# Kernel optimization log

Measured on AMD Instinct MI355X. Metric: run time of the kernel, lower is better.

## Reference

```python
import jax, jax.numpy as jnp
import numpy as np

LOG2_HASHMAP_SIZE = 19
HASHMAP_MASK = np.uint32((1 << LOG2_HASHMAP_SIZE) - 1)
# num_mf_layers=4 -> mf_layer_indices=[2,5,8,11] of the 12-level geometric
# resolution list between base=16 and finest=512
RESOLUTIONS = (30, 80, 210, 512)
PRIMES = (np.uint32(1), np.uint32(11614769), np.uint32(2654435761))
N_POINTS = 2_000_000
N_FEATS = 2

# 8 corner offsets of a 3D voxel, shape [8, 3]
CORNER_OFFSETS = jnp.array([[i, j, k] for i in (0, 1) for j in (0, 1) for k in (0, 1)], dtype=jnp.int32)


def _hash3(coords):
    # coords: [..., 3] int32 grid coordinates -> [...] int32 hash index
    c = coords.astype(jnp.uint32)
    h = (c[..., 0] * PRIMES[0]) ^ (c[..., 1] * PRIMES[1]) ^ (c[..., 2] * PRIMES[2])
    return (h & HASHMAP_MASK).astype(jnp.int32)


def setup_inputs() -> dict:
    key = jax.random.key(0)
    k1, k2 = jax.random.split(key)
    # points inside the unit bounding box
    x = jax.random.uniform(k1, (N_POINTS, 3), dtype=jnp.float32)
    # 4 hash tables, init U(-1e-4, 1e-4) as in nn.init.uniform_
    tables = jax.random.uniform(k2, (len(RESOLUTIONS), 1 << LOG2_HASHMAP_SIZE, N_FEATS),
                                minval=-1e-4, maxval=1e-4, dtype=jnp.float32)
    return {"x": x, "tables": tables}


def reference(x, tables):
    # x: [N, 3] in [0, 1]; tables: [L, 2^19, F]
    outs = []
    for li, res in enumerate(RESOLUTIONS):
        scaled = x * jnp.float32(res)          # [N, 3]
        bottom = jnp.floor(scaled)             # voxel min vertex
        t = scaled - bottom                    # relative position in voxel, [N, 3]
        corners = bottom.astype(jnp.int32)[:, None, :] + CORNER_OFFSETS[None]  # [N, 8, 3]
        idx = _hash3(corners)                  # [N, 8]
        emb = tables[li][idx]                  # gather corner embeddings, [N, 8, F]
        # trilinear weights: prod over dims of (t if offset==1 else 1-t)
        w = jnp.where(CORNER_OFFSETS[None].astype(bool), t[:, None, :], 1.0 - t[:, None, :]).prod(axis=-1)  # [N, 8]
        outs.append(jnp.einsum('nc,ncf->nf', w, emb))  # [N, F]
    return jnp.concatenate(outs, axis=-1)  # [N, L*F] = [N, 8]
```

## Files before the change

kernel.cpp:

```cpp
#include <hip/hip_runtime.h>
#include <stdint.h>

#define LOG2_HASHMAP_SIZE 19
#define HASHMAP_SIZE (1u << LOG2_HASHMAP_SIZE)
#define HASHMAP_MASK (HASHMAP_SIZE - 1u)
#define N_LEVELS 4

__device__ __forceinline__ float2 level_embed_p(float px, float py, float pz,
                                                const float* __restrict__ tables,
                                                int li, float r)
{
    const uint32_t P1 = 11614769u;
    const uint32_t P2 = 2654435761u;

    const float sx = px * r, sy = py * r, sz = pz * r;
    const float bx = floorf(sx), by = floorf(sy), bz = floorf(sz);
    const float tx = sx - bx, ty = sy - by, tz = sz - bz;
    const float ux = 1.0f - tx, uy = 1.0f - ty, uz = 1.0f - tz;

    const uint32_t ix = (uint32_t)(int)bx;
    const uint32_t iy = (uint32_t)(int)by;
    const uint32_t iz = (uint32_t)(int)bz;

    const uint32_t hy0 = iy * P1, hy1 = (iy + 1u) * P1;
    const uint32_t hz0 = iz * P2, hz1 = (iz + 1u) * P2;

    uint32_t S[4];
    float W[4];
    S[0] = hy0 ^ hz0;  W[0] = uy * uz;
    S[1] = hy0 ^ hz1;  W[1] = uy * tz;
    S[2] = hy1 ^ hz0;  W[2] = ty * uz;
    S[3] = hy1 ^ hz1;  W[3] = ty * tz;

    const float* tab = tables + (size_t)li * HASHMAP_SIZE * 2;
    const float2* __restrict__ tab2 = (const float2*)tab;
    const float4* __restrict__ tab4 = (const float4*)tab;

    float f0 = 0.0f, f1 = 0.0f;

    if ((ix & 1u) == 0u) {
        #pragma unroll
        for (int c = 0; c < 4; ++c) {
            const uint32_t h0 = (ix ^ S[c]) & HASHMAP_MASK;
            const float4 v = tab4[h0 >> 1];
            const bool hi = (h0 & 1u);
            const float e0x = hi ? v.z : v.x;
            const float e0y = hi ? v.w : v.y;
            const float e1x = hi ? v.x : v.z;
            const float e1y = hi ? v.y : v.w;
            f0 += W[c] * (ux * e0x + tx * e1x);
            f1 += W[c] * (ux * e0y + tx * e1y);
        }
    } else {
        #pragma unroll
        for (int c = 0; c < 4; ++c) {
            const uint32_t h0 = (ix ^ S[c]) & HASHMAP_MASK;
            const uint32_t h1 = ((ix + 1u) ^ S[c]) & HASHMAP_MASK;
            const float2 e0 = tab2[h0];
            const float2 e1 = tab2[h1];
            f0 += W[c] * (ux * e0.x + tx * e1.x);
            f1 += W[c] * (ux * e0.y + tx * e1.y);
        }
    }
    return make_float2(f0, f1);
}

__global__ __launch_bounds__(256) void pass_ws_kernel(
    const float* __restrict__ x, const float* __restrict__ tables,
    float2* __restrict__ ws, int li, float r, int n)
{
    const int i = blockIdx.x * blockDim.x + threadIdx.x;
    if (i >= n) return;
    const float px = x[3 * (size_t)i + 0];
    const float py = x[3 * (size_t)i + 1];
    const float pz = x[3 * (size_t)i + 2];
    ws[i] = level_embed_p(px, py, pz, tables, li, r);
}

__global__ __launch_bounds__(256) void final_kernel(
    const float* __restrict__ x, const float* __restrict__ tables,
    const float2* __restrict__ ws0, const float2* __restrict__ ws1,
    const float2* __restrict__ ws2, float* __restrict__ out, int n)
{
    const int i = blockIdx.x * blockDim.x + threadIdx.x;
    if (i >= n) return;
    const float px = x[3 * (size_t)i + 0];
    const float py = x[3 * (size_t)i + 1];
    const float pz = x[3 * (size_t)i + 2];
    const float2 e3 = level_embed_p(px, py, pz, tables, 3, 512.0f);
    const float2 e0 = ws0[i];
    const float2 e1 = ws1[i];
    const float2 e2 = ws2[i];
    float4* op = (float4*)(out + 8 * (size_t)i);
    op[0] = make_float4(e0.x, e0.y, e1.x, e1.y);
    op[1] = make_float4(e2.x, e2.y, e3.x, e3.y);
}

__global__ __launch_bounds__(256) void pass_direct_kernel(
    const float* __restrict__ x, const float* __restrict__ tables,
    float* __restrict__ out, int li, float r, int n)
{
    const int i = blockIdx.x * blockDim.x + threadIdx.x;
    if (i >= n) return;
    const float px = x[3 * (size_t)i + 0];
    const float py = x[3 * (size_t)i + 1];
    const float pz = x[3 * (size_t)i + 2];
    const float2 e = level_embed_p(px, py, pz, tables, li, r);
    float2* op = (float2*)(out + 8 * (size_t)i + 2 * li);
    *op = e;
}

extern "C" void kernel_launch(void* const* d_in, const int* in_sizes, int n_in,
                              void* d_out, int out_size, void* d_ws, size_t ws_size,
                              hipStream_t stream) {
    const float* x = (const float*)d_in[0];
    const float* tables = (const float*)d_in[1];
    float* out = (float*)d_out;
    const int n = in_sizes[0] / 3;

    const float res[N_LEVELS] = {30.0f, 80.0f, 210.0f, 512.0f};
    const int block = 256;
    const int grid = (n + block - 1) / block;

    const size_t ws_needed = 3 * (size_t)n * sizeof(float2);
    if (ws_size >= ws_needed) {
        float2* ws = (float2*)d_ws;
        for (int li = 0; li < 3; ++li) {
            pass_ws_kernel<<<grid, block, 0, stream>>>(
                x, tables, ws + (size_t)li * n, li, res[li], n);
        }
        final_kernel<<<grid, block, 0, stream>>>(
            x, tables, ws, ws + (size_t)n, ws + 2 * (size_t)n, out, n);
    } else {
        for (int li = 0; li < N_LEVELS; ++li) {
            pass_direct_kernel<<<grid, block, 0, stream>>>(
                x, tables, out, li, res[li], n);
        }
    }
}
```

Before: 284.2 us.

## Fuse all levels into one persistent kernel with fp16 dense level-0 grid in LDS

Result: slower. 347.7 us (+22.3%).

```diff
diff --git a/kernel.cpp b/kernel.cpp
--- a/kernel.cpp
+++ b/kernel.cpp
@@ -1,10 +1,21 @@
 #include <hip/hip_runtime.h>
+#include <hip/hip_fp16.h>
 #include <stdint.h>
 
 #define LOG2_HASHMAP_SIZE 19
 #define HASHMAP_SIZE (1u << LOG2_HASHMAP_SIZE)
 #define HASHMAP_MASK (HASHMAP_SIZE - 1u)
 #define N_LEVELS 4
+
+#define R0 31
+#define DENSE0_N (R0 * R0 * R0)
+#define DENSE0_BYTES (DENSE0_N * 4)
+
+typedef float v4f __attribute__((ext_vector_type(4)));
+
+__device__ __forceinline__ uint32_t hash3(uint32_t ix, uint32_t iy, uint32_t iz) {
+    return (ix ^ (iy * 11614769u) ^ (iz * 2654435761u)) & HASHMAP_MASK;
+}
 
 __device__ __forceinline__ float2 level_embed_p(float px, float py, float pz,
                                                 const float* __restrict__ tables,
@@ -65,35 +76,71 @@
     return make_float2(f0, f1);
 }
 
-__global__ __launch_bounds__(256) void pass_ws_kernel(
-    const float* __restrict__ x, const float* __restrict__ tables,
-    float2* __restrict__ ws, int li, float r, int n)
+__global__ __launch_bounds__(256) void build_dense0(
+    const float* __restrict__ tables, uint32_t* __restrict__ dense0)
 {
-    const int i = blockIdx.x * blockDim.x + threadIdx.x;
-    if (i >= n) return;
-    const float px = x[3 * (size_t)i + 0];
-    const float py = x[3 * (size_t)i + 1];
-    const float pz = x[3 * (size_t)i + 2];
-    ws[i] = level_embed_p(px, py, pz, tables, li, r);
+    const int v = blockIdx.x * blockDim.x + threadIdx.x;
+    if (v >= DENSE0_N) return;
+    const int vx = v / (R0 * R0);
+    const int rem = v - vx * (R0 * R0);
+    const int vy = rem / R0;
+    const int vz = rem - vy * R0;
+    const uint32_t h = hash3((uint32_t)vx, (uint32_t)vy, (uint32_t)vz);
+    const float2 e = ((const float2*)tables)[h];
+    const __half2 p = __floats2half2_rn(e.x, e.y);
+    dense0[v] = *(const uint32_t*)&p;
 }
 
-__global__ __launch_bounds__(256) void final_kernel(
+extern __shared__ uint32_t s_dense[];
+
+__global__ __launch_bounds__(1024) void fused_kernel(
     const float* __restrict__ x, const float* __restrict__ tables,
-    const float2* __restrict__ ws0, const float2* __restrict__ ws1,
-    const float2* __restrict__ ws2, float* __restrict__ out, int n)
+    const uint32_t* __restrict__ dense0, float* __restrict__ out, int n)
 {
-    const int i = blockIdx.x * blockDim.x + threadIdx.x;
-    if (i >= n) return;
-    const float px = x[3 * (size_t)i + 0];
-    const float py = x[3 * (size_t)i + 1];
-    const float pz = x[3 * (size_t)i + 2];
-    const float2 e3 = level_embed_p(px, py, pz, tables, 3, 512.0f);
-    const float2 e0 = ws0[i];
-    const float2 e1 = ws1[i];
-    const float2 e2 = ws2[i];
-    float4* op = (float4*)(out + 8 * (size_t)i);
-    op[0] = make_float4(e0.x, e0.y, e1.x, e1.y);
-    op[1] = make_float4(e2.x, e2.y, e3.x, e3.y);
+    for (int i = threadIdx.x; i < DENSE0_N; i += 1024)
+        s_dense[i] = dense0[i];
+    __syncthreads();
+
+    const size_t stride = (size_t)gridDim.x * 1024;
+    for (size_t i = (size_t)blockIdx.x * 1024 + threadIdx.x; i < (size_t)n; i += stride) {
+        const float px = __builtin_nontemporal_load(x + 3 * i + 0);
+        const float py = __builtin_nontemporal_load(x + 3 * i + 1);
+        const float pz = __builtin_nontemporal_load(x + 3 * i + 2);
+
+        const float2 e1 = level_embed_p(px, py, pz, tables, 1, 80.0f);
+        const float2 e2 = level_embed_p(px, py, pz, tables, 2, 210.0f);
+        const float2 e3 = level_embed_p(px, py, pz, tables, 3, 512.0f);
+
+        const float sx = px * 30.0f, sy = py * 30.0f, sz = pz * 30.0f;
+        const float bx = floorf(sx), by = floorf(sy), bz = floorf(sz);
+        const float tx = sx - bx, ty = sy - by, tz = sz - bz;
+        const float uxv = 1.0f - tx, uyv = 1.0f - ty, uzv = 1.0f - tz;
+        const int ix = (int)bx, iy = (int)by, iz = (int)bz;
+        const int lin = (ix * R0 + iy) * R0 + iz;
+
+        float f0 = 0.0f, f1 = 0.0f;
+        #pragma unroll
+        for (int dx = 0; dx < 2; ++dx) {
+            const float wx = dx ? tx : uxv;
+            #pragma unroll
+            for (int dy = 0; dy < 2; ++dy) {
+                const float wxy = wx * (dy ? ty : uyv);
+                const int base = lin + (dx * R0 + dy) * R0;
+                const uint32_t p0 = s_dense[base];
+                const uint32_t p1 = s_dense[base + 1];
+                const float2 c0 = __half22float2(*(const __half2*)&p0);
+                const float2 c1 = __half22float2(*(const __half2*)&p1);
+                f0 += wxy * (uzv * c0.x + tz * c1.x);
+                f1 += wxy * (uzv * c0.y + tz * c1.y);
+            }
+        }
+
+        v4f* op = (v4f*)(out + 8 * i);
+        v4f lo = {f0, f1, e1.x, e1.y};
+        v4f hi = {e2.x, e2.y, e3.x, e3.y};
+        __builtin_nontemporal_store(lo, op);
+        __builtin_nontemporal_store(hi, op + 1);
+    }
 }
 
 __global__ __launch_bounds__(256) void pass_direct_kernel(
@@ -118,20 +165,26 @@
     float* out = (float*)d_out;
     const int n = in_sizes[0] / 3;
 
-    const float res[N_LEVELS] = {30.0f, 80.0f, 210.0f, 512.0f};
-    const int block = 256;
-    const int grid = (n + block - 1) / block;
+    bool fused_ok = (ws_size >= (size_t)DENSE0_BYTES);
+    if (fused_ok) {
+        static int attr_ok = -1;
+        if (attr_ok < 0) {
+            attr_ok = (hipFuncSetAttribute(
+                           reinterpret_cast<const void*>(fused_kernel),
+                           hipFuncAttributeMaxDynamicSharedMemorySize,
+                           DENSE0_BYTES) == hipSuccess) ? 1 : 0;
+        }
+        fused_ok = (attr_ok == 1);
+    }
 
-    const size_t ws_needed = 3 * (size_t)n * sizeof(float2);
-    if (ws_size >= ws_needed) {
-        float2* ws = (float2*)d_ws;
-        for (int li = 0; li < 3; ++li) {
-            pass_ws_kernel<<<grid, block, 0, stream>>>(
-                x, tables, ws + (size_t)li * n, li, res[li], n);
-        }
-        final_kernel<<<grid, block, 0, stream>>>(
-            x, tables, ws, ws + (size_t)n, ws + 2 * (size_t)n, out, n);
+    if (fused_ok) {
+        uint32_t* dense0 = (uint32_t*)d_ws;
+        build_dense0<<<(DENSE0_N + 255) / 256, 256, 0, stream>>>(tables, dense0);
+        fused_kernel<<<512, 1024, DENSE0_BYTES, stream>>>(x, tables, dense0, out, n);
     } else {
+        const float res[N_LEVELS] = {30.0f, 80.0f, 210.0f, 512.0f};
+        const int block = 256;
+        const int grid = (n + block - 1) / block;
         for (int li = 0; li < N_LEVELS; ++li) {
             pass_direct_kernel<<<grid, block, 0, stream>>>(
                 x, tables, out, li, res[li], n);
```
